# Performance work log

Measured on AMD Instinct MI355X. Metric: run time of the kernel, lower is better.

The kernel has to match this reference:

```python
import jax, jax.numpy as jnp
import numpy as np

N_NODES = 50000
N_EDGES = 800000
D_IN = 64
D_OUT = 64


def setup_inputs() -> dict:
    key = jax.random.key(0)
    k1, k2, k3, k4 = jax.random.split(key, 4)
    x = jax.random.normal(k1, (N_NODES, D_IN), dtype=jnp.float32)
    W = jax.random.normal(k2, (D_IN, D_OUT), dtype=jnp.float32) / np.sqrt(D_IN)
    bias = jnp.zeros((D_OUT,), dtype=jnp.float32)
    # learned per-edge weights (AdaptiveEdgeWeightGNN.edge_attr, initialized from fixed_values)
    edge_weight = jax.random.uniform(k3, (N_EDGES,), dtype=jnp.float32)
    edge_index = jax.random.randint(k4, (2, N_EDGES), 0, N_NODES, dtype=jnp.int64)
    return {"x": x, "W": W, "bias": bias, "edge_weight": edge_weight, "edge_index": edge_index}


def reference(x, W, bias, edge_weight, edge_index):
    # PyG GCNConv forward: gcn_norm (add self-loops, symmetric normalization
    # using the edge weights), linear transform, gather-scale-scatter, + bias.
    N = x.shape[0]
    row = edge_index[0]  # source nodes
    col = edge_index[1]  # target nodes
    loop = jnp.arange(N, dtype=edge_index.dtype)
    row = jnp.concatenate([row, loop])
    col = jnp.concatenate([col, loop])
    ew = jnp.concatenate([edge_weight, jnp.ones((N,), dtype=edge_weight.dtype)])
    # degree from edge weights scattered onto target nodes
    deg = jax.ops.segment_sum(ew, col, num_segments=N)
    deg_inv_sqrt = jnp.where(deg > 0, jax.lax.rsqrt(deg), 0.0)
    norm = deg_inv_sqrt[row] * ew * deg_inv_sqrt[col]  # [E+N]
    xw = x @ W  # [N, D_OUT]
    msgs = xw[row] * norm[:, None]  # gather + scale
    out = jax.ops.segment_sum(msgs, col, num_segments=N)  # scatter-add
    return out + bias
```

## Files before the change

### kernel.cpp

```cpp
#include <hip/hip_runtime.h>

#define N_NODES 50000
#define N_EDGES 800000
#define D 64
#define NCHUNK 64
#define CHUNK_E (N_EDGES / NCHUNK)
#define NRANGE 4
#define RANGE_N 16384
#define PAD 16
#define REC_CAP (N_EDGES + (PAD - 1) * N_NODES)
#define NB_NODE 196
#define PLACE_BLOCKS (N_EDGES / 256)

__device__ __forceinline__ unsigned short f2bf(float f) {
    unsigned int u = __float_as_uint(f);
    u += 0x7FFFu + ((u >> 16) & 1u);
    return (unsigned short)(u >> 16);
}
__device__ __forceinline__ float bf2f(unsigned short s) {
    return __uint_as_float((unsigned int)s << 16);
}

__global__ __launch_bounds__(1024) void k_hist(const int* __restrict__ col,
                                               unsigned short* __restrict__ part,
                                               unsigned short* __restrict__ lrank) {
    __shared__ unsigned int h[RANGE_N / 2];
    int i = blockIdx.x >> 2;
    int j = blockIdx.x & 3;
    int t = threadIdx.x;
    for (int k = t; k < RANGE_N / 2; k += 1024) h[k] = 0;
    __syncthreads();
    int base = i * CHUNK_E;
    for (int e = base + t; e < base + CHUNK_E; e += 1024) {
        int c = col[e];
        if ((c >> 14) == j) {
            int local = c & (RANGE_N - 1);
            int sh = (local & 1) << 4;
            unsigned int lr = atomicAdd(&h[local >> 1], 1u << sh);
            lrank[e] = (unsigned short)((lr >> sh) & 0xffffu);
        }
    }
    __syncthreads();
    for (int k = t; k < RANGE_N; k += 1024) {
        int n = j * RANGE_N + k;
        if (n < N_NODES)
            part[(size_t)i * N_NODES + n] =
                (unsigned short)((h[k >> 1] >> ((k & 1) << 4)) & 0xffffu);
    }
}

__global__ __launch_bounds__(256) void k_scan(unsigned short* __restrict__ part,
                                              int* __restrict__ start,
                                              int* __restrict__ cnttot,
                                              int* __restrict__ partials) {
    __shared__ int s[256];
    int b = blockIdx.x, t = threadIdx.x;
    int n = b * 256 + t;
    unsigned int run = 0;
    if (n < N_NODES) {
#pragma unroll 8
        for (int i = 0; i < NCHUNK; ++i) {
            size_t idx = (size_t)i * N_NODES + n;
            unsigned int v = part[idx];
            part[idx] = (unsigned short)run;
            run += v;
        }
        cnttot[n] = (int)run;
    }
    int cnt = (n < N_NODES) ? (int)((run + PAD - 1) & ~(unsigned)(PAD - 1)) : 0;
    s[t] = cnt;
    __syncthreads();
    for (int off = 1; off < 256; off <<= 1) {
        int a = (t >= off) ? s[t - off] : 0;
        __syncthreads();
        s[t] += a;
        __syncthreads();
    }
    if (n <= N_NODES) start[n] = s[t] - cnt;
    if (t == 255) partials[b] = s[255];
}

__global__ __launch_bounds__(256) void k_scanfin(int* __restrict__ start,
                                                 const int* __restrict__ partials) {
    __shared__ int red[256];
    int b = blockIdx.x, t = threadIdx.x;
    red[t] = (t < b) ? partials[t] : 0;
    __syncthreads();
    for (int off = 128; off > 0; off >>= 1) {
        if (t < off) red[t] += red[t + off];
        __syncthreads();
    }
    int offset = red[0];
    int n = b * 256 + t;
    if (n <= N_NODES) start[n] += offset;
}

__global__ __launch_bounds__(256) void k_place(const int* __restrict__ ei,
                                               const float* __restrict__ ew,
                                               const int* __restrict__ start,
                                               const int* __restrict__ cnttot,
                                               const unsigned short* __restrict__ part,
                                               const unsigned short* __restrict__ lrank,
                                               int2* __restrict__ rec) {
    int b = blockIdx.x, t = threadIdx.x;
    if (b < PLACE_BLOCKS) {
        int e = b * 256 + t;
        int c = ei[N_EDGES + e];
        int i = e / CHUNK_E;
        int pos = start[c] + (int)part[(size_t)i * N_NODES + c] + (int)lrank[e];
        rec[pos] = make_int2(ei[e], __float_as_int(ew[e]));
    } else {
        int n = (b - PLACE_BLOCKS) * 256 + t;
        if (n < N_NODES) {
            int j = start[n] + cnttot[n];
            int j1 = start[n + 1];
            for (; j < j1; ++j) rec[j] = make_int2(0, 0);
        }
    }
}

__global__ __launch_bounds__(256) void k_deg(const int* __restrict__ start,
                                             const int2* __restrict__ rec,
                                             float* __restrict__ dis) {
    int wave = threadIdx.x >> 6;
    int lane = threadIdx.x & 63;
    int n = blockIdx.x * 4 + wave;
    int j0 = start[n], j1 = start[n + 1];
    float s = 0.0f;
    for (int j = j0 + lane; j < j1; j += 64) s += __int_as_float(rec[j].y);
    for (int off = 32; off > 0; off >>= 1) s += __shfl_down(s, off);
    if (lane == 0) dis[n] = rsqrtf(1.0f + s);
}

__global__ __launch_bounds__(256) void k_xw(const float* __restrict__ x,
                                            const float* __restrict__ W,
                                            const float* __restrict__ dis,
                                            unsigned short* __restrict__ xw16) {
    __shared__ float Ws[64 * 64];
    __shared__ float xs[128 * 68];
    int t = threadIdx.x;
    int r0 = blockIdx.x * 128;

    for (int i = t; i < 1024; i += 256)
        ((float4*)Ws)[i] = ((const float4*)W)[i];
    for (int i = t; i < 2048; i += 256) {
        int row = i >> 4, k4 = i & 15;
        int gr = r0 + row;
        float4 v = make_float4(0.f, 0.f, 0.f, 0.f);
        if (gr < N_NODES) v = ((const float4*)x)[gr * 16 + k4];
        *(float4*)&xs[row * 68 + k4 * 4] = v;
    }
    __syncthreads();

    int cg = t & 15;
    int rg = t >> 4;
    float4 acc[8];
#pragma unroll
    for (int i = 0; i < 8; ++i) acc[i] = make_float4(0.f, 0.f, 0.f, 0.f);

    for (int k4 = 0; k4 < 16; ++k4) {
        float4 xv[8];
#pragma unroll
        for (int i = 0; i < 8; ++i)
            xv[i] = *(const float4*)&xs[(rg + 16 * i) * 68 + k4 * 4];
        float4 w0 = *(const float4*)&Ws[(k4 * 4 + 0) * 64 + cg * 4];
        float4 w1 = *(const float4*)&Ws[(k4 * 4 + 1) * 64 + cg * 4];
        float4 w2 = *(const float4*)&Ws[(k4 * 4 + 2) * 64 + cg * 4];
        float4 w3 = *(const float4*)&Ws[(k4 * 4 + 3) * 64 + cg * 4];
#pragma unroll
        for (int i = 0; i < 8; ++i) {
            acc[i].x = fmaf(xv[i].x, w0.x, acc[i].x); acc[i].y = fmaf(xv[i].x, w0.y, acc[i].y);
            acc[i].z = fmaf(xv[i].x, w0.z, acc[i].z); acc[i].w = fmaf(xv[i].x, w0.w, acc[i].w);
            acc[i].x = fmaf(xv[i].y, w1.x, acc[i].x); acc[i].y = fmaf(xv[i].y, w1.y, acc[i].y);
            acc[i].z = fmaf(xv[i].y, w1.z, acc[i].z); acc[i].w = fmaf(xv[i].y, w1.w, acc[i].w);
            acc[i].x = fmaf(xv[i].z, w2.x, acc[i].x); acc[i].y = fmaf(xv[i].z, w2.y, acc[i].y);
            acc[i].z = fmaf(xv[i].z, w2.z, acc[i].z); acc[i].w = fmaf(xv[i].z, w2.w, acc[i].w);
            acc[i].x = fmaf(xv[i].w, w3.x, acc[i].x); acc[i].y = fmaf(xv[i].w, w3.y, acc[i].y);
            acc[i].z = fmaf(xv[i].w, w3.z, acc[i].z); acc[i].w = fmaf(xv[i].w, w3.w, acc[i].w);
        }
    }

#pragma unroll
    for (int i = 0; i < 8; ++i) {
        int row = r0 + rg + 16 * i;
        if (row < N_NODES) {
            float s = dis[row];
            ushort4 s4 = make_ushort4(f2bf(acc[i].x * s), f2bf(acc[i].y * s),
                                      f2bf(acc[i].z * s), f2bf(acc[i].w * s));
            *(ushort4*)&xw16[row * 64 + cg * 4] = s4;
        }
    }
}

__global__ __launch_bounds__(256) void k_gather(const int* __restrict__ start,
                                                const int2* __restrict__ rec,
                                                const unsigned short* __restrict__ xw16,
                                                const float* __restrict__ dis,
                                                const float* __restrict__ bias,
                                                float* __restrict__ out) {
    int wave = threadIdx.x >> 6;
    int c = threadIdx.x & 63;
    int n = blockIdx.x * 4 + wave;
    float di = dis[n];
    float acc[16];
#pragma unroll
    for (int k = 0; k < 16; ++k) acc[k] = 0.f;
    acc[0] = bf2f(xw16[n * 64 + c]);
    int j = start[n], jend = start[n + 1];
    const int4* rq = (const int4*)(rec + j);
    for (; j < jend; j += 16, rq += 8) {
        int4 q[8];
#pragma unroll
        for (int k = 0; k < 8; ++k) q[k] = rq[k];
        float v[16];
#pragma unroll
        for (int k = 0; k < 8; ++k) {
            v[2 * k]     = bf2f(xw16[q[k].x * 64 + c]);
            v[2 * k + 1] = bf2f(xw16[q[k].z * 64 + c]);
        }
#pragma unroll
        for (int k = 0; k < 8; ++k) {
            acc[2 * k]     = fmaf(v[2 * k],     __int_as_float(q[k].y), acc[2 * k]);
            acc[2 * k + 1] = fmaf(v[2 * k + 1], __int_as_float(q[k].w), acc[2 * k + 1]);
        }
    }
    float a = 0.f;
#pragma unroll
    for (int k = 0; k < 16; ++k) a += acc[k];
    out[n * 64 + c] = fmaf(a, di, bias[c]);
}

extern "C" void kernel_launch(void* const* d_in, const int* in_sizes, int n_in,
                              void* d_out, int out_size, void* d_ws, size_t ws_size,
                              hipStream_t stream) {
    const float* x    = (const float*)d_in[0];
    const float* W    = (const float*)d_in[1];
    const float* bias = (const float*)d_in[2];
    const float* ew   = (const float*)d_in[3];
    const int*   ei   = (const int*)d_in[4];
    float* out = (float*)d_out;

    char* wsb = (char*)d_ws;
    int2*           rec   = (int2*)wsb;
    unsigned short* xw16  = (unsigned short*)(wsb + 12400000);
    unsigned short* lrank = (unsigned short*)(wsb + 18800000);
    unsigned short* part  = (unsigned short*)(wsb + 20400000);
    float*          dis   = (float*)(wsb + 26800000);
    int*            cnttot= (int*)(wsb + 27000000);
    int*            start = (int*)(wsb + 27200000);
    int*            partials = (int*)(wsb + 27400016);

    k_hist<<<NCHUNK * NRANGE, 1024, 0, stream>>>(ei + N_EDGES, part, lrank);
    k_scan<<<NB_NODE, 256, 0, stream>>>(part, start, cnttot, partials);
    k_scanfin<<<NB_NODE, 256, 0, stream>>>(start, partials);
    k_place<<<PLACE_BLOCKS + NB_NODE, 256, 0, stream>>>(ei, ew, start, cnttot, part, lrank, rec);
    k_deg<<<N_NODES / 4, 256, 0, stream>>>(start, rec, dis);
    k_xw<<<(N_NODES + 127) / 128, 256, 0, stream>>>(x, W, dis, xw16);
    k_gather<<<N_NODES / 4, 256, 0, stream>>>(start, rec, xw16, dis, bias, out);
}
```

Measured before the change: 96.04 us.

## Split bf16 feature table into channel halves and gather each half separately

The bf16 xw table is stored as two 32-channel halves, and the gather kernel runs twice, once per half. Each wave now serves two nodes with 32 lanes each. The aim is to shrink the randomly accessed working set per pass to about 3.2 MB so it fits better in cache. In exchange, the edge records are read twice, there is an extra launch, and each gathered row segment is only 64 bytes.

```diff
diff --git a/kernel.cpp b/kernel.cpp
--- a/kernel.cpp
+++ b/kernel.cpp
@@ -135,7 +135,8 @@
 __global__ __launch_bounds__(256) void k_xw(const float* __restrict__ x,
                                             const float* __restrict__ W,
                                             const float* __restrict__ dis,
-                                            unsigned short* __restrict__ xw16) {
+                                            unsigned short* __restrict__ xw_lo,
+                                            unsigned short* __restrict__ xw_hi) {
     __shared__ float Ws[64 * 64];
     __shared__ float xs[128 * 68];
     int t = threadIdx.x;
@@ -187,25 +188,31 @@
             float s = dis[row];
             ushort4 s4 = make_ushort4(f2bf(acc[i].x * s), f2bf(acc[i].y * s),
                                       f2bf(acc[i].z * s), f2bf(acc[i].w * s));
-            *(ushort4*)&xw16[row * 64 + cg * 4] = s4;
+            if (cg < 8) *(ushort4*)&xw_lo[row * 32 + cg * 4] = s4;
+            else        *(ushort4*)&xw_hi[row * 32 + (cg - 8) * 4] = s4;
         }
     }
 }
 
 __global__ __launch_bounds__(256) void k_gather(const int* __restrict__ start,
                                                 const int2* __restrict__ rec,
-                                                const unsigned short* __restrict__ xw16,
+                                                const unsigned short* __restrict__ xwh,
                                                 const float* __restrict__ dis,
                                                 const float* __restrict__ bias,
-                                                float* __restrict__ out) {
-    int wave = threadIdx.x >> 6;
-    int c = threadIdx.x & 63;
-    int n = blockIdx.x * 4 + wave;
+                                                float* __restrict__ out,
+                                                int choff) {
+    int t = threadIdx.x;
+    int wave = t >> 6;
+    int lane = t & 63;
+    int half = lane >> 5;
+    int c = lane & 31;
+    int n = blockIdx.x * 8 + wave * 2 + half;
     float di = dis[n];
+    float bv = bias[choff + c];
     float acc[16];
 #pragma unroll
     for (int k = 0; k < 16; ++k) acc[k] = 0.f;
-    acc[0] = bf2f(xw16[n * 64 + c]);
+    acc[0] = bf2f(xwh[n * 32 + c]);
     int j = start[n], jend = start[n + 1];
     const int4* rq = (const int4*)(rec + j);
     for (; j < jend; j += 16, rq += 8) {
@@ -215,8 +222,8 @@
         float v[16];
 #pragma unroll
         for (int k = 0; k < 8; ++k) {
-            v[2 * k]     = bf2f(xw16[q[k].x * 64 + c]);
-            v[2 * k + 1] = bf2f(xw16[q[k].z * 64 + c]);
+            v[2 * k]     = bf2f(xwh[q[k].x * 32 + c]);
+            v[2 * k + 1] = bf2f(xwh[q[k].z * 32 + c]);
         }
 #pragma unroll
         for (int k = 0; k < 8; ++k) {
@@ -227,7 +234,7 @@
     float a = 0.f;
 #pragma unroll
     for (int k = 0; k < 16; ++k) a += acc[k];
-    out[n * 64 + c] = fmaf(a, di, bias[c]);
+    out[n * 64 + choff + c] = fmaf(a, di, bv);
 }
 
 extern "C" void kernel_launch(void* const* d_in, const int* in_sizes, int n_in,
@@ -242,7 +249,8 @@
 
     char* wsb = (char*)d_ws;
     int2*           rec   = (int2*)wsb;
-    unsigned short* xw16  = (unsigned short*)(wsb + 12400000);
+    unsigned short* xw_lo = (unsigned short*)(wsb + 12400000);
+    unsigned short* xw_hi = (unsigned short*)(wsb + 15600000);
     unsigned short* lrank = (unsigned short*)(wsb + 18800000);
     unsigned short* part  = (unsigned short*)(wsb + 20400000);
     float*          dis   = (float*)(wsb + 26800000);
@@ -255,6 +263,7 @@
     k_scanfin<<<NB_NODE, 256, 0, stream>>>(start, partials);
     k_place<<<PLACE_BLOCKS + NB_NODE, 256, 0, stream>>>(ei, ew, start, cnttot, part, lrank, rec);
     k_deg<<<N_NODES / 4, 256, 0, stream>>>(start, rec, dis);
-    k_xw<<<(N_NODES + 127) / 128, 256, 0, stream>>>(x, W, dis, xw16);
-    k_gather<<<N_NODES / 4, 256, 0, stream>>>(start, rec, xw16, dis, bias, out);
-}
+    k_xw<<<(N_NODES + 127) / 128, 256, 0, stream>>>(x, W, dis, xw_lo, xw_hi);
+    k_gather<<<N_NODES / 8, 256, 0, stream>>>(start, rec, xw_lo, dis, bias, out, 0);
+    k_gather<<<N_NODES / 8, 256, 0, stream>>>(start, rec, xw_hi, dis, bias, out, 32);
+}
```

Measured after the change: 102.8 us. 1.07x slower.
